# Performance work log

Measured on AMD Instinct MI355X. Metric: run time of the kernel, lower is better.

Reference implementation:

```python
import jax, jax.numpy as jnp
import numpy as np
import math

J = 50000      # number of atomic environments
NSP = 4        # number of species
NMAX = 8       # max radial
LMAX = 6       # max angular


def setup_inputs() -> dict:
    key = jax.random.key(0)
    keys = jax.random.split(key, LMAX + 1)
    inp = {}
    for l in range(LMAX + 1):
        inp[f"se_{l}"] = jax.random.normal(keys[l], (J, NSP, NMAX, 2 * l + 1), dtype=jnp.float32)
    return inp


def _powerspectrum(se_list):
    Jn, nsp, nmax, _ = se_list[0].shape
    A = nsp * nmax
    diag_ids = np.arange(A)
    iu0, iu1 = np.triu_indices(A, k=1)
    parts = []
    for l, se in enumerate(se_list):
        se = se.reshape(Jn, A, 2 * l + 1)
        # symmetric Gram over the combined (species, radial) channel, contracted over m
        outer = jnp.einsum('iam,ibm->iab', se, se) / math.sqrt(2 * l + 1)  # [J, A, A]
        diag = outer[:, diag_ids, diag_ids]                # [J, A]
        upper = math.sqrt(2.0) * outer[:, iu0, iu1]        # [J, A*(A-1)/2]
        parts.append(jnp.concatenate([diag, upper], axis=1))
    # concatenating per-l blocks in order l=0..lmax matches PS.view(J, -1)
    return jnp.concatenate(parts, axis=1)


def reference(se_0, se_1, se_2, se_3, se_4, se_5, se_6):
    se_list = [se_0, se_1, se_2, se_3, se_4, se_5, se_6]
    ps = _powerspectrum(se_list)                           # [J, D]
    # torch.nn.functional.normalize(..., dim=1): x / max(||x||_2, 1e-12)
    norm = jnp.linalg.norm(ps, axis=1, keepdims=True)
    return ps / jnp.maximum(norm, 1e-12)
```

## Files before the change

### kernel.cpp

```cpp
#include <hip/hip_runtime.h>

#define NL 7
#define NA 32
#define PERL 528
#define NF 3696
#define RSH 24
#define SQRT2f 1.41421356237309515f

typedef __attribute__((ext_vector_type(8))) short bf16x8;
typedef __attribute__((ext_vector_type(16))) float f32x16;
typedef __attribute__((ext_vector_type(4))) float nf4;
typedef float f32x4u __attribute__((ext_vector_type(4), aligned(4)));

__device__ __forceinline__ unsigned f2bf(float f) {
    union { float f; unsigned u; } c; c.f = f;
    return (c.u + 0x7fffu + ((c.u >> 16) & 1u)) >> 16;
}

#define STAGE_CASE(L, SE, SGL) {                                                \
    constexpr int m21 = 2 * (L) + 1;                                            \
    const float* src = (SE) + (size_t)j * (32 * m21) + a * m21;                 \
    float buf[16];                                                              \
    _Pragma("unroll") for (int i = 0; i < 16; ++i) buf[i] = 0.0f;               \
    if constexpr (m21 < 4) {                                                    \
        _Pragma("unroll") for (int m = 0; m < m21; ++m) buf[m] = src[m];        \
    } else {                                                                    \
        constexpr int nf = m21 >> 2;                                            \
        _Pragma("unroll") for (int q = 0; q < nf; ++q) {                        \
            f32x4u v = *(const f32x4u*)(src + 4 * q);                           \
            _Pragma("unroll") for (int i = 0; i < 4; ++i) buf[4 * q + i] = v[i];\
        }                                                                       \
        {   f32x4u v = *(const f32x4u*)(src + m21 - 4);                         \
            _Pragma("unroll") for (int i = 0; i < 4; ++i) buf[m21 - 4 + i] = v[i]; } \
    }                                                                           \
    unsigned pk[8];                                                             \
    _Pragma("unroll") for (int p = 0; p < 8; ++p)                               \
        pk[p] = f2bf(buf[2 * p] * (SGL)) | (f2bf(buf[2 * p + 1] * (SGL)) << 16);\
    unsigned short* rowp = Th + ((L) * 32 + a) * RSH;                           \
    *(uint4*)(rowp)     = make_uint4(pk[0], pk[1], pk[2], pk[3]);               \
    *(uint4*)(rowp + 8) = make_uint4(pk[4], pk[5], pk[6], pk[7]);               \
}

__global__ __launch_bounds__(256) void ps_kernel(
    const float* __restrict__ se0, const float* __restrict__ se1,
    const float* __restrict__ se2, const float* __restrict__ se3,
    const float* __restrict__ se4, const float* __restrict__ se5,
    const float* __restrict__ se6, float* __restrict__ out)
{
    __shared__ __align__(16) float LB[NF];
    __shared__ float s_wsum[4];
    __shared__ float s_inv;
    unsigned short* Th = (unsigned short*)LB;

    const int j   = blockIdx.x;
    const int tid = threadIdx.x;

    if (tid < 224) {
        const int a = tid & 31;
        switch (tid >> 5) {
            case 0: STAGE_CASE(0, se0, 1.0f);           break;
            case 1: STAGE_CASE(1, se1, 0.7598356857f);  break;
            case 2: STAGE_CASE(2, se2, 0.6687403050f);  break;
            case 3: STAGE_CASE(3, se3, 0.6147881526f);  break;
            case 4: STAGE_CASE(4, se4, 0.5773502692f);  break;
            case 5: STAGE_CASE(5, se5, 0.5491004040f);  break;
            case 6: STAGE_CASE(6, se6, 0.5266403878f);  break;
        }
    }
    __syncthreads();

    const int wv   = tid >> 6;
    const int lane = tid & 63;
    const int row  = lane & 31;
    const int hoff = (lane >> 5) * 8;

    const int lA = wv;
    const int lB = wv + 4;

    f32x16 accA, accB;
    #pragma unroll
    for (int r = 0; r < 16; ++r) { accA[r] = 0.0f; accB[r] = 0.0f; }

    {
        const bf16x8 fA = *(const bf16x8*)(Th + (lA * 32 + row) * RSH + hoff);
        accA = __builtin_amdgcn_mfma_f32_32x32x16_bf16(fA, fA, accA, 0, 0, 0);
    }
    if (lB < NL) {
        const bf16x8 fB = *(const bf16x8*)(Th + (lB * 32 + row) * RSH + hoff);
        accB = __builtin_amdgcn_mfma_f32_32x32x16_bf16(fB, fB, accB, 0, 0, 0);
    }

    float ssq = 0.0f;
    #pragma unroll
    for (int r = 0; r < 16; ++r) ssq += accA[r] * accA[r] + accB[r] * accB[r];

    #pragma unroll
    for (int off = 32; off >= 1; off >>= 1) ssq += __shfl_down(ssq, off, 64);
    if (lane == 0) s_wsum[wv] = ssq;
    __syncthreads();

    if (tid == 0) {
        const float tot = s_wsum[0] + s_wsum[1] + s_wsum[2] + s_wsum[3];
        s_inv = 1.0f / fmaxf(sqrtf(tot), 1e-12f);
    }

    const int c     = lane & 31;
    const int hi4   = (lane >> 5) * 4;
    const int ubase = 32 + (c * (63 - c)) / 2 - c - 1;

    {
        float* ol = LB + lA * PERL;
        #pragma unroll
        for (int r = 0; r < 16; ++r) {
            const int rw = (r & 3) + 8 * (r >> 2) + hi4;
            if (rw >= c) {
                const bool d = (rw == c);
                ol[d ? c : (ubase + rw)] = d ? accA[r] : accA[r] * SQRT2f;
            }
        }
    }
    if (lB < NL) {
        float* ol = LB + lB * PERL;
        #pragma unroll
        for (int r = 0; r < 16; ++r) {
            const int rw = (r & 3) + 8 * (r >> 2) + hi4;
            if (rw >= c) {
                const bool d = (rw == c);
                ol[d ? c : (ubase + rw)] = d ? accB[r] : accB[r] * SQRT2f;
            }
        }
    }
    __syncthreads();

    const float inv = s_inv;
    const nf4* ob4 = (const nf4*)LB;
    nf4* op4 = (nf4*)(out + (size_t)j * NF);
    #pragma unroll
    for (int k = 0; k < 4; ++k) {
        const int q = tid + k * 256;
        if (q < 924) {
            nf4 v = ob4[q];
            v *= inv;
            __builtin_nontemporal_store(v, &op4[q]);
        }
    }
}

extern "C" void kernel_launch(void* const* d_in, const int* in_sizes, int n_in,
                              void* d_out, int out_size, void* d_ws, size_t ws_size,
                              hipStream_t stream) {
    const float* se0 = (const float*)d_in[0];
    const float* se1 = (const float*)d_in[1];
    const float* se2 = (const float*)d_in[2];
    const float* se3 = (const float*)d_in[3];
    const float* se4 = (const float*)d_in[4];
    const float* se5 = (const float*)d_in[5];
    const float* se6 = (const float*)d_in[6];
    float* out = (float*)d_out;

    const int J = in_sizes[0] / NA;
    ps_kernel<<<J, 256, 0, stream>>>(se0, se1, se2, se3, se4, se5, se6, out);
}
```

Before: 202.7 us.

## Stage per-wave angular blocks locally and fold normalization into the Gram scatter

Staging is remapped so each wave loads and converts exactly the two l-blocks its own MFMAs consume. The half-waves split the low and high l values, so the block-wide barrier after staging becomes a wave barrier. The 1/sqrt(2l+1) scaling moves from the bf16 input to the fp32 accumulators, along with the 1/norm factor. Every thread now computes the norm, which removes the single-thread s_inv step and the multiply in the final copy loop. Packing uses the hardware v_cvt_pk_bf16_f32 instruction. Since the kernel is dominated by global output traffic, the saved synchronization and ALU work may matter little.

After: 198.5 us (median of 2 runs). 1.02x faster.

```diff
diff --git a/kernel.cpp b/kernel.cpp
--- a/kernel.cpp
+++ b/kernel.cpp
@@ -7,38 +7,76 @@
 #define RSH 24
 #define SQRT2f 1.41421356237309515f
 
-typedef __attribute__((ext_vector_type(8))) short bf16x8;
-typedef __attribute__((ext_vector_type(16))) float f32x16;
-typedef __attribute__((ext_vector_type(4))) float nf4;
+typedef short bf16x8 __attribute__((ext_vector_type(8)));
+typedef float f32x16 __attribute__((ext_vector_type(16)));
+typedef unsigned uint4v __attribute__((ext_vector_type(4)));
 typedef float f32x4u __attribute__((ext_vector_type(4), aligned(4)));
 
-__device__ __forceinline__ unsigned f2bf(float f) {
-    union { float f; unsigned u; } c; c.f = f;
-    return (c.u + 0x7fffu + ((c.u >> 16) & 1u)) >> 16;
-}
-
-#define STAGE_CASE(L, SE, SGL) {                                                \
-    constexpr int m21 = 2 * (L) + 1;                                            \
-    const float* src = (SE) + (size_t)j * (32 * m21) + a * m21;                 \
-    float buf[16];                                                              \
-    _Pragma("unroll") for (int i = 0; i < 16; ++i) buf[i] = 0.0f;               \
-    if constexpr (m21 < 4) {                                                    \
-        _Pragma("unroll") for (int m = 0; m < m21; ++m) buf[m] = src[m];        \
-    } else {                                                                    \
-        constexpr int nf = m21 >> 2;                                            \
-        _Pragma("unroll") for (int q = 0; q < nf; ++q) {                        \
-            f32x4u v = *(const f32x4u*)(src + 4 * q);                           \
-            _Pragma("unroll") for (int i = 0; i < 4; ++i) buf[4 * q + i] = v[i];\
-        }                                                                       \
-        {   f32x4u v = *(const f32x4u*)(src + m21 - 4);                         \
-            _Pragma("unroll") for (int i = 0; i < 4; ++i) buf[m21 - 4 + i] = v[i]; } \
-    }                                                                           \
-    unsigned pk[8];                                                             \
-    _Pragma("unroll") for (int p = 0; p < 8; ++p)                               \
-        pk[p] = f2bf(buf[2 * p] * (SGL)) | (f2bf(buf[2 * p + 1] * (SGL)) << 16);\
-    unsigned short* rowp = Th + ((L) * 32 + a) * RSH;                           \
-    *(uint4*)(rowp)     = make_uint4(pk[0], pk[1], pk[2], pk[3]);               \
-    *(uint4*)(rowp + 8) = make_uint4(pk[4], pk[5], pk[6], pk[7]);               \
+__device__ __forceinline__ unsigned cvtpk(float lo, float hi) {
+    unsigned r;
+    asm("v_cvt_pk_bf16_f32 %0, %1, %2" : "=v"(r) : "v"(lo), "v"(hi));
+    return r;
+}
+
+template<int L>
+__device__ __forceinline__ void stage_lo(const float* __restrict__ se, int j, int a,
+                                         unsigned short* __restrict__ Th) {
+    constexpr int m21 = 2 * L + 1;
+    const float* rowp = se + (size_t)j * (32 * m21) + a * m21;
+    float v[8];
+    #pragma unroll
+    for (int i = 0; i < 8; ++i) v[i] = 0.0f;
+    if constexpr (m21 == 1) { v[0] = rowp[0]; }
+    else if constexpr (m21 == 3) {
+        f32x4u t = *(const f32x4u*)rowp;
+        v[0] = t[0]; v[1] = t[1]; v[2] = t[2];
+    } else if constexpr (m21 == 5) {
+        f32x4u t = *(const f32x4u*)rowp;
+        v[0] = t[0]; v[1] = t[1]; v[2] = t[2]; v[3] = t[3];
+        v[4] = rowp[4];
+    } else {
+        f32x4u t0 = *(const f32x4u*)rowp;
+        f32x4u t1 = *(const f32x4u*)(rowp + 3);
+        v[0] = t0[0]; v[1] = t0[1]; v[2] = t0[2];
+        v[3] = t1[0]; v[4] = t1[1]; v[5] = t1[2]; v[6] = t1[3];
+    }
+    unsigned pk[4];
+    #pragma unroll
+    for (int p = 0; p < 4; ++p) pk[p] = (2 * p < m21) ? cvtpk(v[2 * p], v[2 * p + 1]) : 0u;
+    unsigned short* rp = Th + (L * 32 + a) * RSH;
+    *(uint4*)rp       = make_uint4(pk[0], pk[1], pk[2], pk[3]);
+    *(uint4*)(rp + 8) = make_uint4(0u, 0u, 0u, 0u);
+}
+
+template<int L>
+__device__ __forceinline__ void stage_hi(const float* __restrict__ se, int j, int a,
+                                         unsigned short* __restrict__ Th) {
+    constexpr int m21 = 2 * L + 1;
+    const float* rowp = se + (size_t)j * (32 * m21) + a * m21;
+    float v[16];
+    #pragma unroll
+    for (int i = 0; i < 16; ++i) v[i] = 0.0f;
+    {
+        f32x4u t0 = *(const f32x4u*)rowp;
+        f32x4u t1 = *(const f32x4u*)(rowp + 4);
+        #pragma unroll
+        for (int i = 0; i < 4; ++i) { v[i] = t0[i]; v[4 + i] = t1[i]; }
+    }
+    if constexpr (m21 == 9) { v[8] = rowp[8]; }
+    else if constexpr (m21 == 11) {
+        f32x4u t = *(const f32x4u*)(rowp + 7);
+        v[8] = t[1]; v[9] = t[2]; v[10] = t[3];
+    } else {
+        f32x4u t = *(const f32x4u*)(rowp + 8);
+        v[8] = t[0]; v[9] = t[1]; v[10] = t[2]; v[11] = t[3];
+        v[12] = rowp[12];
+    }
+    unsigned pk[8];
+    #pragma unroll
+    for (int p = 0; p < 8; ++p) pk[p] = (2 * p < m21) ? cvtpk(v[2 * p], v[2 * p + 1]) : 0u;
+    unsigned short* rp = Th + (L * 32 + a) * RSH;
+    *(uint4*)rp       = make_uint4(pk[0], pk[1], pk[2], pk[3]);
+    *(uint4*)(rp + 8) = make_uint4(pk[4], pk[5], pk[6], pk[7]);
 }
 
 __global__ __launch_bounds__(256) void ps_kernel(
@@ -49,31 +87,36 @@
 {
     __shared__ __align__(16) float LB[NF];
     __shared__ float s_wsum[4];
-    __shared__ float s_inv;
     unsigned short* Th = (unsigned short*)LB;
 
-    const int j   = blockIdx.x;
-    const int tid = threadIdx.x;
-
-    if (tid < 224) {
-        const int a = tid & 31;
-        switch (tid >> 5) {
-            case 0: STAGE_CASE(0, se0, 1.0f);           break;
-            case 1: STAGE_CASE(1, se1, 0.7598356857f);  break;
-            case 2: STAGE_CASE(2, se2, 0.6687403050f);  break;
-            case 3: STAGE_CASE(3, se3, 0.6147881526f);  break;
-            case 4: STAGE_CASE(4, se4, 0.5773502692f);  break;
-            case 5: STAGE_CASE(5, se5, 0.5491004040f);  break;
-            case 6: STAGE_CASE(6, se6, 0.5266403878f);  break;
-        }
-    }
-    __syncthreads();
-
+    const int j    = blockIdx.x;
+    const int tid  = threadIdx.x;
     const int wv   = tid >> 6;
     const int lane = tid & 63;
+
+    {
+        const int a = lane & 31;
+        if (lane < 32) {
+            switch (wv) {
+                case 0:  stage_lo<0>(se0, j, a, Th); break;
+                case 1:  stage_lo<1>(se1, j, a, Th); break;
+                case 2:  stage_lo<2>(se2, j, a, Th); break;
+                default: stage_lo<3>(se3, j, a, Th); break;
+            }
+        } else {
+            switch (wv) {
+                case 0:  stage_hi<4>(se4, j, a, Th); break;
+                case 1:  stage_hi<5>(se5, j, a, Th); break;
+                case 2:  stage_hi<6>(se6, j, a, Th); break;
+                default: break;
+            }
+        }
+    }
+    __builtin_amdgcn_wave_barrier();
+    asm volatile("" ::: "memory");
+
     const int row  = lane & 31;
     const int hoff = (lane >> 5) * 8;
-
     const int lA = wv;
     const int lB = wv + 4;
 
@@ -90,57 +133,58 @@
         accB = __builtin_amdgcn_mfma_f32_32x32x16_bf16(fB, fB, accB, 0, 0, 0);
     }
 
-    float ssq = 0.0f;
-    #pragma unroll
-    for (int r = 0; r < 16; ++r) ssq += accA[r] * accA[r] + accB[r] * accB[r];
+    const float rsA = rsqrtf((float)(2 * lA + 1));
+    const float rsB = rsqrtf((float)(2 * lB + 1));
+    float sA = 0.0f, sB = 0.0f;
+    #pragma unroll
+    for (int r = 0; r < 16; ++r) { sA += accA[r] * accA[r]; sB += accB[r] * accB[r]; }
+    float ssq = sA * (rsA * rsA) + ((lB < NL) ? sB * (rsB * rsB) : 0.0f);
 
     #pragma unroll
     for (int off = 32; off >= 1; off >>= 1) ssq += __shfl_down(ssq, off, 64);
     if (lane == 0) s_wsum[wv] = ssq;
     __syncthreads();
 
-    if (tid == 0) {
-        const float tot = s_wsum[0] + s_wsum[1] + s_wsum[2] + s_wsum[3];
-        s_inv = 1.0f / fmaxf(sqrtf(tot), 1e-12f);
-    }
+    const float tot = s_wsum[0] + s_wsum[1] + s_wsum[2] + s_wsum[3];
+    const float inv = 1.0f / fmaxf(sqrtf(tot), 1e-12f);
 
     const int c     = lane & 31;
     const int hi4   = (lane >> 5) * 4;
     const int ubase = 32 + (c * (63 - c)) / 2 - c - 1;
 
     {
+        const float dsc = rsA * inv, usc = dsc * SQRT2f;
         float* ol = LB + lA * PERL;
         #pragma unroll
         for (int r = 0; r < 16; ++r) {
             const int rw = (r & 3) + 8 * (r >> 2) + hi4;
             if (rw >= c) {
                 const bool d = (rw == c);
-                ol[d ? c : (ubase + rw)] = d ? accA[r] : accA[r] * SQRT2f;
+                ol[d ? c : (ubase + rw)] = accA[r] * (d ? dsc : usc);
             }
         }
     }
     if (lB < NL) {
+        const float dsc = rsB * inv, usc = dsc * SQRT2f;
         float* ol = LB + lB * PERL;
         #pragma unroll
         for (int r = 0; r < 16; ++r) {
             const int rw = (r & 3) + 8 * (r >> 2) + hi4;
             if (rw >= c) {
                 const bool d = (rw == c);
-                ol[d ? c : (ubase + rw)] = d ? accB[r] : accB[r] * SQRT2f;
+                ol[d ? c : (ubase + rw)] = accB[r] * (d ? dsc : usc);
             }
         }
     }
     __syncthreads();
 
-    const float inv = s_inv;
-    const nf4* ob4 = (const nf4*)LB;
-    nf4* op4 = (nf4*)(out + (size_t)j * NF);
+    const uint4v* ob4 = (const uint4v*)LB;
+    uint4v* op4 = (uint4v*)(out + (size_t)j * NF);
     #pragma unroll
     for (int k = 0; k < 4; ++k) {
         const int q = tid + k * 256;
         if (q < 924) {
-            nf4 v = ob4[q];
-            v *= inv;
+            uint4v v = ob4[q];
             __builtin_nontemporal_store(v, &op4[q]);
         }
     }
```
